# Kernel tuning notes

Measured on AMD Instinct MI355X. Metric: run time of the kernel, lower is better.

Reference implementation:

```python
import jax, jax.numpy as jnp
import numpy as np

B, S, D, H, F, E = 4, 1024, 1024, 16, 4096, 8
HD = D // H  # head dim


def setup_inputs() -> dict:
    key = jax.random.key(0)
    ks = jax.random.split(key, 8)
    p = lambda k, shp: jax.random.normal(k, shp, jnp.float32) * 0.02
    return {
        "x": jax.random.normal(ks[0], (B, S, D), jnp.float32),
        "mask": jnp.ones((B, S), jnp.int32),
        "in_proj_w": p(ks[1], (3 * D, D)),
        "in_proj_b": jnp.zeros((3 * D,), jnp.float32),
        "out_proj_w": p(ks[2], (D, D)),
        "out_proj_b": jnp.zeros((D,), jnp.float32),
        "ln1_g": jnp.ones((D,), jnp.float32),
        "ln1_b": jnp.zeros((D,), jnp.float32),
        "ln2_g": jnp.ones((D,), jnp.float32),
        "ln2_b": jnp.zeros((D,), jnp.float32),
        "gate_w": p(ks[3], (E, D)),
        "gate_b": jnp.zeros((E,), jnp.float32),
        "w1": p(ks[4], (E, F, D)),
        "b1": jnp.zeros((E, F), jnp.float32),
        "w2": p(ks[5], (E, D, F)),
        "b2": jnp.zeros((E, D), jnp.float32),
    }


def _layernorm(x, g, b, eps=1e-5):
    m = x.mean(-1, keepdims=True)
    v = ((x - m) ** 2).mean(-1, keepdims=True)
    return (x - m) / jnp.sqrt(v + eps) * g + b


def _mha(x, key_pad, in_proj_w, in_proj_b, out_proj_w, out_proj_b):
    # combined QKV projection as in torch nn.MultiheadAttention
    qkv = x @ in_proj_w.T + in_proj_b  # (B,S,3D)
    q, k, v = jnp.split(qkv, 3, axis=-1)
    def heads(t):
        return t.reshape(B, S, H, HD).transpose(0, 2, 1, 3)  # (B,H,S,HD)
    q, k, v = heads(q), heads(k), heads(v)
    scores = jnp.einsum("bhqd,bhkd->bhqk", q, k) / jnp.sqrt(jnp.float32(HD))
    scores = jnp.where(key_pad[:, None, None, :], -1e30, scores)
    attn = jax.nn.softmax(scores, axis=-1)
    out = jnp.einsum("bhqk,bhkd->bhqd", attn, v)  # (B,H,S,HD)
    out = out.transpose(0, 2, 1, 3).reshape(B, S, D)
    return out @ out_proj_w.T + out_proj_b


def _moe(x, gate_w, gate_b, w1, b1, w2, b2):
    logits = x @ gate_w.T + gate_b            # (B,S,E)
    probs = jax.nn.softmax(logits, axis=-1)
    # dense all-expert FFN (faithful to original: every expert computed)
    h = jax.nn.relu(jnp.einsum("bsd,efd->bsef", x, w1) + b1)   # (B,S,E,F)
    all_out = jnp.einsum("bsef,edf->bsed", h, w2) + b2          # (B,S,E,D)
    top_vals, top_idx = jax.lax.top_k(probs, 2)                 # (B,S,2)
    weights = top_vals / (top_vals.sum(-1, keepdims=True) + 1e-9)
    sel = jnp.take_along_axis(all_out, top_idx[..., None], axis=2)  # (B,S,2,D)
    return (sel * weights[..., None]).sum(axis=2)


def reference(x, mask, in_proj_w, in_proj_b, out_proj_w, out_proj_b,
              ln1_g, ln1_b, ln2_g, ln2_b, gate_w, gate_b, w1, b1, w2, b2):
    key_pad = mask == 0  # (B,S) bool
    attn_out = _mha(x, key_pad, in_proj_w, in_proj_b, out_proj_w, out_proj_b)
    x1 = _layernorm(x + attn_out, ln1_g, ln1_b)
    ff = _moe(x1, gate_w, gate_b, w1, b1, w2, b2)
    return _layernorm(x1 + ff, ln2_g, ln2_b)
```

## Files before the change

### kernel.cpp

```cpp
#include <hip/hip_runtime.h>

typedef __attribute__((ext_vector_type(8))) short bf16x8;
typedef __attribute__((ext_vector_type(4))) float f32x4;

#define DEV __device__ __forceinline__

static constexpr int Bb = 4, Sq = 1024, Dd = 1024, Hh = 16, HDd = 64, Ff = 4096, Ee = 8;
static constexpr int Nn = Bb * Sq;
static constexpr int TD = 3 * Dd;
static constexpr int PMAX = 2 * Nn + Ee * 128;

DEV unsigned short f2bf(float x) {
  union { float f; unsigned u; } c; c.f = x;
  unsigned r = c.u + 0x7FFFu + ((c.u >> 16) & 1u);
  return (unsigned short)(r >> 16);
}

typedef const __attribute__((address_space(1))) unsigned int* gas_t;
typedef __attribute__((address_space(3))) unsigned int* las_t;
DEV void gload16(const void* g, void* l) {
  __builtin_amdgcn_global_load_lds((gas_t)g, (las_t)l, 16, 0, 0);
}

__global__ __launch_bounds__(256) void cvt_kernel(const float* __restrict__ in,
                                                  unsigned short* __restrict__ out) {
  int i = blockIdx.x * 256 + threadIdx.x;
  const float4 a = *(const float4*)(in + (size_t)i * 8);
  const float4 b = *(const float4*)(in + (size_t)i * 8 + 4);
  union { uint4 u; unsigned short s[8]; } pk;
  pk.s[0] = f2bf(a.x); pk.s[1] = f2bf(a.y); pk.s[2] = f2bf(a.z); pk.s[3] = f2bf(a.w);
  pk.s[4] = f2bf(b.x); pk.s[5] = f2bf(b.y); pk.s[6] = f2bf(b.z); pk.s[7] = f2bf(b.w);
  *(uint4*)(out + (size_t)i * 8) = pk.u;
}

template <int EPI>
__global__ __launch_bounds__(256) void gemm_bt(
    const unsigned short* __restrict__ A, const unsigned short* __restrict__ Bw,
    const float* __restrict__ bias, void* __restrict__ o0, void* __restrict__ o1,
    void* __restrict__ o2, int M, int Ncols, int K,
    const int* __restrict__ poff) {
  int bx, by;
  {
    const int gx = gridDim.x, nwg = gx * gridDim.y;
    int orig = blockIdx.y * gx + blockIdx.x;
    int q = nwg >> 3, r = nwg & 7;
    int xcd = orig & 7, lin = orig >> 3;
    int wg = (xcd < r ? xcd * (q + 1) : r * (q + 1) + (xcd - r) * q) + lin;
    bx = wg % gx; by = wg / gx;
  }
  const int m0 = bx * 128;
  int e = 0;
  if constexpr (EPI >= 2) {
    if (m0 >= poff[Ee]) return;
#pragma unroll
    for (int k = 1; k < Ee; ++k) if (m0 >= poff[k]) e = k;
  } else {
    if (m0 >= M) return;
  }
  const int n0 = by * 128;
  const unsigned short* Bptr = Bw + (size_t)e * Ncols * K;
  const float* biasptr = bias + e * Ncols;

  __shared__ __align__(128) unsigned short As[3 * 128 * 32];
  __shared__ __align__(128) unsigned short Bs[3 * 128 * 32];

  const int tid = threadIdx.x;
  const int lane = tid & 63, wid = tid >> 6;
  const int wm = wid >> 1, wn = wid & 1;
  const int lr = lane & 15, lk = lane >> 4;

  const char* aSrc[2]; const char* bSrc[2];
  int dOff[2];
#pragma unroll
  for (int it = 0; it < 2; ++it) {
    int b = it * 4096 + tid * 16;
    int r = b >> 6;
    int colb = (b & 63) ^ (((r >> 1) & 3) << 4);
    aSrc[it] = (const char*)(A + (size_t)(m0 + r) * K) + colb;
    bSrc[it] = (const char*)(Bptr + (size_t)(n0 + r) * K) + colb;
    dOff[it] = it * 4096 + wid * 1024;
  }
  int aOff[4], bOff[4];
#pragma unroll
  for (int i = 0; i < 4; ++i) {
    int ra = wm * 64 + i * 16 + lr;
    aOff[i] = ra * 32 + ((lk ^ ((ra >> 1) & 3)) << 3);
    int rb = wn * 64 + i * 16 + lr;
    bOff[i] = rb * 32 + ((lk ^ ((rb >> 1) & 3)) << 3);
  }

  auto STAGE = [&](int t, int buf) {
#pragma unroll
    for (int it = 0; it < 2; ++it) {
      gload16(aSrc[it] + (size_t)t * 64, (char*)As + buf * 8192 + dOff[it]);
      gload16(bSrc[it] + (size_t)t * 64, (char*)Bs + buf * 8192 + dOff[it]);
    }
  };

  f32x4 acc[4][4] = {};
  const int NT = K >> 5;

  STAGE(0, 0);
  STAGE(1, 1);
  int cb = 0;
  int sb = 2;
  for (int t = 0; t < NT; ++t) {
    if (t + 1 < NT) asm volatile("s_waitcnt vmcnt(4)" ::: "memory");
    else            asm volatile("s_waitcnt vmcnt(0)" ::: "memory");
    __builtin_amdgcn_sched_barrier(0);
    __builtin_amdgcn_s_barrier();
    __builtin_amdgcn_sched_barrier(0);
    if (t + 2 < NT) STAGE(t + 2, sb);
    const unsigned short* Ab = As + cb * 4096;
    const unsigned short* Bb2 = Bs + cb * 4096;
    bf16x8 af[4], bfv[4];
#pragma unroll
    for (int mi = 0; mi < 4; ++mi) af[mi] = *(const bf16x8*)&Ab[aOff[mi]];
#pragma unroll
    for (int ni = 0; ni < 4; ++ni) bfv[ni] = *(const bf16x8*)&Bb2[bOff[ni]];
#pragma unroll
    for (int mi = 0; mi < 4; ++mi)
#pragma unroll
      for (int ni = 0; ni < 4; ++ni)
        acc[mi][ni] = __builtin_amdgcn_mfma_f32_16x16x32_bf16(af[mi], bfv[ni], acc[mi][ni], 0, 0, 0);
    cb = (cb == 2) ? 0 : cb + 1;
    sb = (sb == 2) ? 0 : sb + 1;
  }

#pragma unroll
  for (int ni = 0; ni < 4; ++ni) {
    const int col = n0 + wn * 64 + ni * 16 + lr;
    const float bv = biasptr[col];
#pragma unroll
    for (int mi = 0; mi < 4; ++mi) {
#pragma unroll
      for (int i = 0; i < 4; ++i) {
        const int mloc = wm * 64 + mi * 16 + lk * 4 + i;
        float v = acc[mi][ni][i] + bv;
        if constexpr (EPI == 0) {
          int t = m0 + mloc;
          int which = col >> 10, jj = col & 1023, hh = jj >> 6, hd = jj & 63;
          int bb = t >> 10, s = t & 1023;
          unsigned short* dst = (which == 0) ? (unsigned short*)o0
                              : (which == 1) ? (unsigned short*)o1 : (unsigned short*)o2;
          dst[((size_t)(bb * Hh + hh) * Sq + s) * HDd + hd] = f2bf(v);
        } else if constexpr (EPI == 1) {
          ((float*)o0)[(size_t)(m0 + mloc) * Dd + col] = v;
        } else if constexpr (EPI == 2) {
          ((unsigned short*)o0)[(size_t)(m0 + mloc) * Ff + col] = f2bf(fmaxf(v, 0.f));
        } else {
          ((float*)o0)[(size_t)(m0 + mloc) * Dd + col] = v;
        }
      }
    }
  }
}

__global__ __launch_bounds__(256) void attn_kernel(
    const unsigned short* __restrict__ qb, const unsigned short* __restrict__ kb,
    const unsigned short* __restrict__ vb, const int* __restrict__ mask,
    unsigned short* __restrict__ attnb) {
  const int qt = blockIdx.x, h = blockIdx.y, b = blockIdx.z;
  const unsigned short* Q = qb + (size_t)(b * Hh + h) * Sq * HDd;
  const unsigned short* Kg = kb + (size_t)(b * Hh + h) * Sq * HDd;
  const unsigned short* Vg = vb + (size_t)(b * Hh + h) * Sq * HDd;

  __shared__ unsigned short Qs[64 * 72], Ks[64 * 72], Vt[64 * 72], Ps[64 * 72];
  __shared__ float Ssm[64 * 65];
  __shared__ float mS[64], lS[64], aS[64];
  __shared__ int mk[64];

  const int tid = threadIdx.x, lane = tid & 63, wid = tid >> 6;
  const int lr = lane & 15, lk = lane >> 4;

#pragma unroll
  for (int it = 0; it < 2; ++it) {
    int c = tid + it * 256; int r = c >> 3, kc = (c & 7) * 8;
    *(uint4*)&Qs[r * 72 + kc] = *(const uint4*)(Q + (size_t)(qt * 64 + r) * 64 + kc);
  }
  if (tid < 64) { mS[tid] = -1e30f; lS[tid] = 0.f; }

  f32x4 oacc[4] = {};

  for (int kt = 0; kt < 16; ++kt) {
    __syncthreads();
#pragma unroll
    for (int it = 0; it < 2; ++it) {
      int c = tid + it * 256; int r = c >> 3, kc = (c & 7) * 8;
      *(uint4*)&Ks[r * 72 + kc] = *(const uint4*)(Kg + (size_t)(kt * 64 + r) * 64 + kc);
    }
    {
      int kk = tid >> 2, hg = (tid & 3) * 16;
      union { uint4 u[2]; unsigned short s[16]; } tv;
      tv.u[0] = *(const uint4*)(Vg + (size_t)(kt * 64 + kk) * 64 + hg);
      tv.u[1] = *(const uint4*)(Vg + (size_t)(kt * 64 + kk) * 64 + hg + 8);
#pragma unroll
      for (int j = 0; j < 16; ++j) Vt[(hg + j) * 72 + kk] = tv.s[j];
    }
    if (tid < 64) mk[tid] = mask[b * Sq + kt * 64 + tid];
    __syncthreads();

    f32x4 sacc[4] = {};
#pragma unroll
    for (int ks = 0; ks < 2; ++ks) {
      bf16x8 aq = *(const bf16x8*)&Qs[(wid * 16 + lr) * 72 + ks * 32 + lk * 8];
#pragma unroll
      for (int ni = 0; ni < 4; ++ni) {
        bf16x8 bk = *(const bf16x8*)&Ks[(ni * 16 + lr) * 72 + ks * 32 + lk * 8];
        sacc[ni] = __builtin_amdgcn_mfma_f32_16x16x32_bf16(aq, bk, sacc[ni], 0, 0, 0);
      }
    }
#pragma unroll
    for (int ni = 0; ni < 4; ++ni)
#pragma unroll
      for (int i = 0; i < 4; ++i) {
        int r = wid * 16 + lk * 4 + i, cc = ni * 16 + lr;
        float v = sacc[ni][i] * 0.125f;
        if (mk[cc] == 0) v = -1e30f;
        Ssm[r * 65 + cc] = v;
      }
    __syncthreads();
    {
      int r = tid >> 2, cg = (tid & 3) * 16;
      float xv[16];
#pragma unroll
      for (int j = 0; j < 16; ++j) xv[j] = Ssm[r * 65 + cg + j];
      float mx = xv[0];
#pragma unroll
      for (int j = 1; j < 16; ++j) mx = fmaxf(mx, xv[j]);
      mx = fmaxf(mx, __shfl_xor(mx, 1));
      mx = fmaxf(mx, __shfl_xor(mx, 2));
      float mprev = mS[r];
      float mnew = fmaxf(mprev, mx);
      float sum = 0.f;
      union { uint4 u[2]; unsigned short s[16]; } pb;
#pragma unroll
      for (int j = 0; j < 16; ++j) {
        float pv = expf(xv[j] - mnew);
        sum += pv; pb.s[j] = f2bf(pv);
      }
      sum += __shfl_xor(sum, 1);
      sum += __shfl_xor(sum, 2);
      *(uint4*)&Ps[r * 72 + cg] = pb.u[0];
      *(uint4*)&Ps[r * 72 + cg + 8] = pb.u[1];
      if ((tid & 3) == 0) {
        float alpha = expf(mprev - mnew);
        mS[r] = mnew; aS[r] = alpha; lS[r] = lS[r] * alpha + sum;
      }
    }
    __syncthreads();
#pragma unroll
    for (int ni = 0; ni < 4; ++ni)
#pragma unroll
      for (int i = 0; i < 4; ++i)
        oacc[ni][i] *= aS[wid * 16 + lk * 4 + i];
#pragma unroll
    for (int ks = 0; ks < 2; ++ks) {
      bf16x8 ap = *(const bf16x8*)&Ps[(wid * 16 + lr) * 72 + ks * 32 + lk * 8];
#pragma unroll
      for (int ni = 0; ni < 4; ++ni) {
        bf16x8 bv = *(const bf16x8*)&Vt[(ni * 16 + lr) * 72 + ks * 32 + lk * 8];
        oacc[ni] = __builtin_amdgcn_mfma_f32_16x16x32_bf16(ap, bv, oacc[ni], 0, 0, 0);
      }
    }
  }
  __syncthreads();
#pragma unroll
  for (int ni = 0; ni < 4; ++ni)
#pragma unroll
    for (int i = 0; i < 4; ++i) {
      int r = wid * 16 + lk * 4 + i;
      int q = qt * 64 + r;
      float v = oacc[ni][i] / lS[r];
      attnb[((size_t)(b * Sq + q)) * Dd + h * 64 + ni * 16 + lr] = f2bf(v);
    }
}

__global__ __launch_bounds__(256) void ln_kernel(
    const float* __restrict__ a, const float* __restrict__ b2,
    const float* __restrict__ g, const float* __restrict__ beta,
    float* __restrict__ outf, unsigned short* __restrict__ outb) {
  const int t = blockIdx.x, tid = threadIdx.x;
  float4 v = *(const float4*)(a + (size_t)t * Dd + tid * 4);
  {
    float4 u = *(const float4*)(b2 + (size_t)t * Dd + tid * 4);
    v.x += u.x; v.y += u.y; v.z += u.z; v.w += u.w;
  }
  const int lane = tid & 63, wid = tid >> 6;
  float s = v.x + v.y + v.z + v.w;
  for (int sh = 1; sh < 64; sh <<= 1) s += __shfl_xor(s, sh);
  __shared__ float red[4], red2[4];
  if (lane == 0) red[wid] = s;
  __syncthreads();
  float mean = (red[0] + red[1] + red[2] + red[3]) * (1.f / Dd);
  float dx = v.x - mean, dy = v.y - mean, dz = v.z - mean, dw = v.w - mean;
  float q = dx * dx + dy * dy + dz * dz + dw * dw;
  for (int sh = 1; sh < 64; sh <<= 1) q += __shfl_xor(q, sh);
  if (lane == 0) red2[wid] = q;
  __syncthreads();
  float var = (red2[0] + red2[1] + red2[2] + red2[3]) * (1.f / Dd);
  float rstd = rsqrtf(var + 1e-5f);
  float4 gg = *(const float4*)(g + tid * 4);
  float4 bb = *(const float4*)(beta + tid * 4);
  float4 o;
  o.x = dx * rstd * gg.x + bb.x;
  o.y = dy * rstd * gg.y + bb.y;
  o.z = dz * rstd * gg.z + bb.z;
  o.w = dw * rstd * gg.w + bb.w;
  if (outf) *(float4*)(outf + (size_t)t * Dd + tid * 4) = o;
  if (outb) {
    ushort4 pk; pk.x = f2bf(o.x); pk.y = f2bf(o.y); pk.z = f2bf(o.z); pk.w = f2bf(o.w);
    *(ushort4*)(outb + (size_t)t * Dd + tid * 4) = pk;
  }
}

__global__ __launch_bounds__(256) void ln2_kernel(
    const float* __restrict__ x1f, const float* __restrict__ ffp,
    const int* __restrict__ inv, const float* __restrict__ wtok,
    const float* __restrict__ g, const float* __restrict__ beta,
    float* __restrict__ out) {
  const int t = blockIdx.x, tid = threadIdx.x;
  const int i0 = inv[2 * t], i1 = inv[2 * t + 1];
  const float w0 = wtok[2 * t], w1 = wtok[2 * t + 1];
  float4 v = *(const float4*)(x1f + (size_t)t * Dd + tid * 4);
  float4 u0 = *(const float4*)(ffp + (size_t)i0 * Dd + tid * 4);
  float4 u1 = *(const float4*)(ffp + (size_t)i1 * Dd + tid * 4);
  v.x += w0 * u0.x + w1 * u1.x; v.y += w0 * u0.y + w1 * u1.y;
  v.z += w0 * u0.z + w1 * u1.z; v.w += w0 * u0.w + w1 * u1.w;
  const int lane = tid & 63, wid = tid >> 6;
  float s = v.x + v.y + v.z + v.w;
  for (int sh = 1; sh < 64; sh <<= 1) s += __shfl_xor(s, sh);
  __shared__ float red[4], red2[4];
  if (lane == 0) red[wid] = s;
  __syncthreads();
  float mean = (red[0] + red[1] + red[2] + red[3]) * (1.f / Dd);
  float dx = v.x - mean, dy = v.y - mean, dz = v.z - mean, dw = v.w - mean;
  float q = dx * dx + dy * dy + dz * dz + dw * dw;
  for (int sh = 1; sh < 64; sh <<= 1) q += __shfl_xor(q, sh);
  if (lane == 0) red2[wid] = q;
  __syncthreads();
  float var = (red2[0] + red2[1] + red2[2] + red2[3]) * (1.f / Dd);
  float rstd = rsqrtf(var + 1e-5f);
  float4 gg = *(const float4*)(g + tid * 4);
  float4 bb = *(const float4*)(beta + tid * 4);
  float4 o;
  o.x = dx * rstd * gg.x + bb.x;
  o.y = dy * rstd * gg.y + bb.y;
  o.z = dz * rstd * gg.z + bb.z;
  o.w = dw * rstd * gg.w + bb.w;
  *(float4*)(out + (size_t)t * Dd + tid * 4) = o;
}

__global__ __launch_bounds__(256) void route_kernel(
    const float* __restrict__ x1f, const float* __restrict__ gw, const float* __restrict__ gb,
    int* __restrict__ cnt, int* __restrict__ tokslot, float* __restrict__ wtok) {
  __shared__ float gws[Ee * Dd];
  const int tid = threadIdx.x;
#pragma unroll
  for (int it = 0; it < 8; ++it) {
    int idx = (tid + it * 256) * 4;
    *(float4*)&gws[idx] = *(const float4*)(gw + idx);
  }
  __syncthreads();
  const int lane = tid & 63, wid = tid >> 6;
  for (int it = 0; it < 16; ++it) {
    int t = blockIdx.x * 64 + wid * 16 + it;
    float acc[Ee] = {};
    for (int i = 0; i < 16; ++i) {
      float xv = x1f[(size_t)t * Dd + i * 64 + lane];
#pragma unroll
      for (int e = 0; e < Ee; ++e) acc[e] += xv * gws[e * Dd + i * 64 + lane];
    }
#pragma unroll
    for (int e = 0; e < Ee; ++e) {
      float vv = acc[e];
      for (int sh = 1; sh < 64; sh <<= 1) vv += __shfl_xor(vv, sh);
      acc[e] = vv;
    }
    if (lane == 0) {
      float lg[Ee];
#pragma unroll
      for (int e = 0; e < Ee; ++e) lg[e] = acc[e] + gb[e];
      float m = lg[0];
#pragma unroll
      for (int e = 1; e < Ee; ++e) m = fmaxf(m, lg[e]);
      float p[Ee], ssum = 0.f;
#pragma unroll
      for (int e = 0; e < Ee; ++e) { p[e] = expf(lg[e] - m); ssum += p[e]; }
      int e0 = 0;
#pragma unroll
      for (int e = 1; e < Ee; ++e) if (p[e] > p[e0]) e0 = e;
      int e1 = -1;
#pragma unroll
      for (int e = 0; e < Ee; ++e) {
        if (e == e0) continue;
        if (e1 < 0 || p[e] > p[e1]) e1 = e;
      }
      float v0 = p[e0] / ssum, v1 = p[e1] / ssum;
      float wsum = v0 + v1 + 1e-9f;
      wtok[t * 2] = v0 / wsum; wtok[t * 2 + 1] = v1 / wsum;
      int p0 = atomicAdd(&cnt[e0], 1);
      tokslot[e0 * Nn + p0] = t * 2;
      int p1 = atomicAdd(&cnt[e1], 1);
      tokslot[e1 * Nn + p1] = t * 2 + 1;
    }
  }
}

__global__ void offsets_kernel(const int* __restrict__ cnt, int* __restrict__ poff) {
  if (threadIdx.x == 0) {
    int s = 0;
    for (int e = 0; e < Ee; ++e) { poff[e] = s; s += (cnt[e] + 127) & ~127; }
    poff[Ee] = s;
  }
}

__global__ __launch_bounds__(256) void pack_kernel(
    const unsigned short* __restrict__ x1b, const int* __restrict__ tokslot,
    const int* __restrict__ cnt, const int* __restrict__ poff,
    unsigned short* __restrict__ xg, int* __restrict__ inv) {
  const int tid = threadIdx.x;
  const int g = blockIdx.x * 8 + (tid >> 5);
  const int l = tid & 31;
  if (g >= poff[Ee]) return;
  int e = 0;
#pragma unroll
  for (int k = 1; k < Ee; ++k) if (g >= poff[k]) e = k;
  const int pos = g - poff[e];
  uint4* dst = (uint4*)(xg + (size_t)g * Dd);
  if (pos < cnt[e]) {
    const int ent = tokslot[e * Nn + pos];
    if (l == 0) inv[ent] = g;
    const uint4* src = (const uint4*)(x1b + (size_t)(ent >> 1) * Dd);
#pragma unroll
    for (int j = 0; j < 4; ++j) dst[l + j * 32] = src[l + j * 32];
  } else {
    const uint4 z = make_uint4(0, 0, 0, 0);
#pragma unroll
    for (int j = 0; j < 4; ++j) dst[l + j * 32] = z;
  }
}

extern "C" void kernel_launch(void* const* d_in, const int* in_sizes, int n_in,
                              void* d_out, int out_size, void* d_ws, size_t ws_size,
                              hipStream_t stream) {
  const float* x   = (const float*)d_in[0];
  const int*   msk = (const int*)d_in[1];
  const float* ipw = (const float*)d_in[2];
  const float* ipb = (const float*)d_in[3];
  const float* opw = (const float*)d_in[4];
  const float* opb = (const float*)d_in[5];
  const float* g1  = (const float*)d_in[6];
  const float* be1 = (const float*)d_in[7];
  const float* g2  = (const float*)d_in[8];
  const float* be2 = (const float*)d_in[9];
  const float* gw  = (const float*)d_in[10];
  const float* gb  = (const float*)d_in[11];
  const float* w1  = (const float*)d_in[12];
  const float* b1  = (const float*)d_in[13];
  const float* w2  = (const float*)d_in[14];
  const float* b2  = (const float*)d_in[15];
  float* out = (float*)d_out;

  char* p = (char*)d_ws;
  auto carve = [&](size_t bytes) { char* r = p; p += (bytes + 255) & ~(size_t)255; return r; };
  unsigned short* xb   = (unsigned short*)carve((size_t)Nn * Dd * 2);
  unsigned short* qb   = (unsigned short*)carve((size_t)Nn * Dd * 2);
  unsigned short* kb   = (unsigned short*)carve((size_t)Nn * Dd * 2);
  unsigned short* vb   = (unsigned short*)carve((size_t)Nn * Dd * 2);
  float* proj          = (float*)carve((size_t)Nn * Dd * 4);
  float* x1f           = (float*)carve((size_t)Nn * Dd * 4);
  unsigned short* x1b  = (unsigned short*)carve((size_t)Nn * Dd * 2);
  unsigned short* xg   = (unsigned short*)carve((size_t)PMAX * Dd * 2);
  float* ffp           = (float*)carve((size_t)PMAX * Dd * 4);
  unsigned short* hbuf = (unsigned short*)carve((size_t)PMAX * Ff * 2);
  unsigned short* wbuf = (unsigned short*)carve((size_t)Ee * Ff * Dd * 2);
  int* cnt             = (int*)carve(64);
  int* poff            = (int*)carve(64);
  int* tokslot         = (int*)carve((size_t)Ee * Nn * 4);
  float* wtok          = (float*)carve((size_t)2 * Nn * 4);
  int* inv             = (int*)carve((size_t)2 * Nn * 4);
  unsigned short* attnb = xb;

  cvt_kernel<<<Nn * Dd / 2048, 256, 0, stream>>>(x, xb);
  cvt_kernel<<<TD * Dd / 2048, 256, 0, stream>>>(ipw, wbuf);
  gemm_bt<0><<<dim3(Nn / 128, TD / 128), 256, 0, stream>>>(
      xb, wbuf, ipb, qb, kb, vb, Nn, TD, Dd, nullptr);
  attn_kernel<<<dim3(Sq / 64, Hh, Bb), 256, 0, stream>>>(qb, kb, vb, msk, attnb);
  cvt_kernel<<<Dd * Dd / 2048, 256, 0, stream>>>(opw, wbuf);
  gemm_bt<1><<<dim3(Nn / 128, Dd / 128), 256, 0, stream>>>(
      attnb, wbuf, opb, proj, nullptr, nullptr, Nn, Dd, Dd, nullptr);
  ln_kernel<<<Nn, 256, 0, stream>>>(x, proj, g1, be1, x1f, x1b);
  hipMemsetAsync(cnt, 0, 64, stream);
  route_kernel<<<Nn / 64, 256, 0, stream>>>(x1f, gw, gb, cnt, tokslot, wtok);
  offsets_kernel<<<1, 64, 0, stream>>>(cnt, poff);
  pack_kernel<<<PMAX / 8, 256, 0, stream>>>(x1b, tokslot, cnt, poff, xg, inv);
  cvt_kernel<<<Ee * Ff * Dd / 2048, 256, 0, stream>>>(w1, wbuf);
  gemm_bt<2><<<dim3(PMAX / 128, Ff / 128), 256, 0, stream>>>(
      xg, wbuf, b1, hbuf, nullptr, nullptr, PMAX, Ff, Dd, poff);
  cvt_kernel<<<Ee * Dd * Ff / 2048, 256, 0, stream>>>(w2, wbuf);
  gemm_bt<3><<<dim3(PMAX / 128, Dd / 128), 256, 0, stream>>>(
      hbuf, wbuf, b2, ffp, nullptr, nullptr, PMAX, Dd, Ff, poff);
  ln2_kernel<<<Nn, 256, 0, stream>>>(x1f, ffp, inv, wtok, g2, be2, out);
}
```

Before: 627.5 us.

## Use 256-row tiles with 512-thread blocks for the MoE expert GEMMs

Adds a new gemm256 kernel for the two grouped expert GEMMs. It uses 256-row M tiles with 256- or 128-wide N tiles, a 64-wide K step, double-buffered LDS and 8 waves per block, in place of the 128x128 tile kernel with K step 32. Per-expert padding goes from 128 to 256 rows to match. This is meant to raise data reuse per block and cut the number of barriers and loads per MFMA, at the cost of more padding rows, fewer blocks and higher LDS and register use per block.

```diff
diff --git a/kernel.cpp b/kernel.cpp
--- a/kernel.cpp
+++ b/kernel.cpp
@@ -8,7 +8,7 @@
 static constexpr int Bb = 4, Sq = 1024, Dd = 1024, Hh = 16, HDd = 64, Ff = 4096, Ee = 8;
 static constexpr int Nn = Bb * Sq;
 static constexpr int TD = 3 * Dd;
-static constexpr int PMAX = 2 * Nn + Ee * 128;
+static constexpr int PMAX = 2 * Nn + Ee * 256;
 
 DEV unsigned short f2bf(float x) {
   union { float f; unsigned u; } c; c.f = x;
@@ -33,12 +33,19 @@
   *(uint4*)(out + (size_t)i * 8) = pk.u;
 }
 
-template <int EPI>
-__global__ __launch_bounds__(256) void gemm_bt(
+template <int EPI, int TN>
+__global__ __launch_bounds__(512) void gemm256(
     const unsigned short* __restrict__ A, const unsigned short* __restrict__ Bw,
-    const float* __restrict__ bias, void* __restrict__ o0, void* __restrict__ o1,
-    void* __restrict__ o2, int M, int Ncols, int K,
-    const int* __restrict__ poff) {
+    const float* __restrict__ bias, void* __restrict__ o0,
+    int Ncols, int K, const int* __restrict__ poff) {
+  constexpr int NW_N = TN / 64;
+  constexpr int NW_M = 8 / NW_N;
+  constexpr int RM = 256 / NW_M;
+  constexpr int MI = RM / 16;
+  constexpr int NB = TN / 64;
+  constexpr int ASZ = 256 * 64;
+  constexpr int BSZ = TN * 64;
+
   int bx, by;
   {
     const int gx = gridDim.x, nwg = gx * gridDim.y;
@@ -48,18 +55,136 @@
     int wg = (xcd < r ? xcd * (q + 1) : r * (q + 1) + (xcd - r) * q) + lin;
     bx = wg % gx; by = wg / gx;
   }
-  const int m0 = bx * 128;
+  const int m0 = bx * 256;
+  if (m0 >= poff[Ee]) return;
   int e = 0;
-  if constexpr (EPI >= 2) {
-    if (m0 >= poff[Ee]) return;
-#pragma unroll
-    for (int k = 1; k < Ee; ++k) if (m0 >= poff[k]) e = k;
-  } else {
-    if (m0 >= M) return;
-  }
-  const int n0 = by * 128;
+#pragma unroll
+  for (int k = 1; k < Ee; ++k) if (m0 >= poff[k]) e = k;
+  const int n0 = by * TN;
   const unsigned short* Bptr = Bw + (size_t)e * Ncols * K;
   const float* biasptr = bias + e * Ncols;
+
+  __shared__ __align__(128) unsigned short As[2 * ASZ];
+  __shared__ __align__(128) unsigned short Bs[2 * BSZ];
+
+  const int tid = threadIdx.x;
+  const int lane = tid & 63, wid = tid >> 6;
+  const int wm = wid / NW_N, wn = wid % NW_N;
+  const int lr = lane & 15, lk = lane >> 4;
+
+  const char* aSrc[4]; const char* bSrc[NB];
+  int aDstOff[4], bDstOff[NB];
+#pragma unroll
+  for (int it = 0; it < 4; ++it) {
+    int b = it * 8192 + tid * 16;
+    int r = b >> 7;
+    int colb = (b & 127) ^ ((r & 7) << 4);
+    aSrc[it] = (const char*)(A + (size_t)(m0 + r) * K) + colb;
+    aDstOff[it] = it * 8192 + wid * 1024;
+  }
+#pragma unroll
+  for (int it = 0; it < NB; ++it) {
+    int b = it * 8192 + tid * 16;
+    int r = b >> 7;
+    int colb = (b & 127) ^ ((r & 7) << 4);
+    bSrc[it] = (const char*)(Bptr + (size_t)(n0 + r) * K) + colb;
+    bDstOff[it] = it * 8192 + wid * 1024;
+  }
+  int aOff[2][MI], bOff[2][4];
+#pragma unroll
+  for (int ks = 0; ks < 2; ++ks) {
+#pragma unroll
+    for (int i = 0; i < MI; ++i) {
+      int ra = wm * RM + i * 16 + lr;
+      aOff[ks][i] = ra * 64 + (((ks * 4 + lk) ^ (ra & 7)) << 3);
+    }
+#pragma unroll
+    for (int i = 0; i < 4; ++i) {
+      int rb = wn * 64 + i * 16 + lr;
+      bOff[ks][i] = rb * 64 + (((ks * 4 + lk) ^ (rb & 7)) << 3);
+    }
+  }
+
+  f32x4 acc[MI][4] = {};
+  const int NT = K >> 6;
+
+  auto STAGE = [&](int t, int buf) {
+#pragma unroll
+    for (int it = 0; it < 4; ++it)
+      gload16(aSrc[it] + (size_t)t * 128, (char*)As + buf * (ASZ * 2) + aDstOff[it]);
+#pragma unroll
+    for (int it = 0; it < NB; ++it)
+      gload16(bSrc[it] + (size_t)t * 128, (char*)Bs + buf * (BSZ * 2) + bDstOff[it]);
+  };
+
+  STAGE(0, 0);
+  for (int t = 0; t < NT; ++t) {
+    __builtin_amdgcn_s_barrier();
+    __builtin_amdgcn_sched_barrier(0);
+    if (t + 1 < NT) {
+      STAGE(t + 1, (t + 1) & 1);
+      if constexpr (TN == 256) asm volatile("s_waitcnt vmcnt(8)" ::: "memory");
+      else                     asm volatile("s_waitcnt vmcnt(6)" ::: "memory");
+    } else {
+      asm volatile("s_waitcnt vmcnt(0)" ::: "memory");
+    }
+    __builtin_amdgcn_sched_barrier(0);
+    __builtin_amdgcn_s_barrier();
+    __builtin_amdgcn_sched_barrier(0);
+    const unsigned short* Ab = As + (t & 1) * ASZ;
+    const unsigned short* Bb2 = Bs + (t & 1) * BSZ;
+#pragma unroll
+    for (int ks = 0; ks < 2; ++ks) {
+      bf16x8 af[MI], bfv[4];
+#pragma unroll
+      for (int mi = 0; mi < MI; ++mi) af[mi] = *(const bf16x8*)&Ab[aOff[ks][mi]];
+#pragma unroll
+      for (int ni = 0; ni < 4; ++ni) bfv[ni] = *(const bf16x8*)&Bb2[bOff[ks][ni]];
+#pragma unroll
+      for (int mi = 0; mi < MI; ++mi)
+#pragma unroll
+        for (int ni = 0; ni < 4; ++ni)
+          acc[mi][ni] = __builtin_amdgcn_mfma_f32_16x16x32_bf16(af[mi], bfv[ni], acc[mi][ni], 0, 0, 0);
+    }
+  }
+
+#pragma unroll
+  for (int ni = 0; ni < 4; ++ni) {
+    const int col = n0 + wn * 64 + ni * 16 + lr;
+    const float bv = biasptr[col];
+#pragma unroll
+    for (int mi = 0; mi < MI; ++mi) {
+#pragma unroll
+      for (int i = 0; i < 4; ++i) {
+        const int grow = m0 + wm * RM + mi * 16 + lk * 4 + i;
+        float v = acc[mi][ni][i] + bv;
+        if constexpr (EPI == 2) {
+          ((unsigned short*)o0)[(size_t)grow * Ff + col] = f2bf(fmaxf(v, 0.f));
+        } else {
+          ((float*)o0)[(size_t)grow * Dd + col] = v;
+        }
+      }
+    }
+  }
+}
+
+template <int EPI>
+__global__ __launch_bounds__(256) void gemm_bt(
+    const unsigned short* __restrict__ A, const unsigned short* __restrict__ Bw,
+    const float* __restrict__ bias, void* __restrict__ o0, void* __restrict__ o1,
+    void* __restrict__ o2, int M, int Ncols, int K) {
+  int bx, by;
+  {
+    const int gx = gridDim.x, nwg = gx * gridDim.y;
+    int orig = blockIdx.y * gx + blockIdx.x;
+    int q = nwg >> 3, r = nwg & 7;
+    int xcd = orig & 7, lin = orig >> 3;
+    int wg = (xcd < r ? xcd * (q + 1) : r * (q + 1) + (xcd - r) * q) + lin;
+    bx = wg % gx; by = wg / gx;
+  }
+  const int m0 = bx * 128;
+  if (m0 >= M) return;
+  const int n0 = by * 128;
 
   __shared__ __align__(128) unsigned short As[3 * 128 * 32];
   __shared__ __align__(128) unsigned short Bs[3 * 128 * 32];
@@ -77,7 +202,7 @@
     int r = b >> 6;
     int colb = (b & 63) ^ (((r >> 1) & 3) << 4);
     aSrc[it] = (const char*)(A + (size_t)(m0 + r) * K) + colb;
-    bSrc[it] = (const char*)(Bptr + (size_t)(n0 + r) * K) + colb;
+    bSrc[it] = (const char*)(Bw + (size_t)(n0 + r) * K) + colb;
     dOff[it] = it * 4096 + wid * 1024;
   }
   int aOff[4], bOff[4];
@@ -102,8 +227,7 @@
 
   STAGE(0, 0);
   STAGE(1, 1);
-  int cb = 0;
-  int sb = 2;
+  int cb = 0, sb = 2;
   for (int t = 0; t < NT; ++t) {
     if (t + 1 < NT) asm volatile("s_waitcnt vmcnt(4)" ::: "memory");
     else            asm volatile("s_waitcnt vmcnt(0)" ::: "memory");
@@ -130,7 +254,7 @@
 #pragma unroll
   for (int ni = 0; ni < 4; ++ni) {
     const int col = n0 + wn * 64 + ni * 16 + lr;
-    const float bv = biasptr[col];
+    const float bv = bias[col];
 #pragma unroll
     for (int mi = 0; mi < 4; ++mi) {
 #pragma unroll
@@ -144,10 +268,6 @@
           unsigned short* dst = (which == 0) ? (unsigned short*)o0
                               : (which == 1) ? (unsigned short*)o1 : (unsigned short*)o2;
           dst[((size_t)(bb * Hh + hh) * Sq + s) * HDd + hd] = f2bf(v);
-        } else if constexpr (EPI == 1) {
-          ((float*)o0)[(size_t)(m0 + mloc) * Dd + col] = v;
-        } else if constexpr (EPI == 2) {
-          ((unsigned short*)o0)[(size_t)(m0 + mloc) * Ff + col] = f2bf(fmaxf(v, 0.f));
         } else {
           ((float*)o0)[(size_t)(m0 + mloc) * Dd + col] = v;
         }
@@ -410,7 +530,7 @@
 __global__ void offsets_kernel(const int* __restrict__ cnt, int* __restrict__ poff) {
   if (threadIdx.x == 0) {
     int s = 0;
-    for (int e = 0; e < Ee; ++e) { poff[e] = s; s += (cnt[e] + 127) & ~127; }
+    for (int e = 0; e < Ee; ++e) { poff[e] = s; s += (cnt[e] + 255) & ~255; }
     poff[Ee] = s;
   }
 }
@@ -485,21 +605,21 @@
   cvt_kernel<<<Nn * Dd / 2048, 256, 0, stream>>>(x, xb);
   cvt_kernel<<<TD * Dd / 2048, 256, 0, stream>>>(ipw, wbuf);
   gemm_bt<0><<<dim3(Nn / 128, TD / 128), 256, 0, stream>>>(
-      xb, wbuf, ipb, qb, kb, vb, Nn, TD, Dd, nullptr);
+      xb, wbuf, ipb, qb, kb, vb, Nn, TD, Dd);
   attn_kernel<<<dim3(Sq / 64, Hh, Bb), 256, 0, stream>>>(qb, kb, vb, msk, attnb);
   cvt_kernel<<<Dd * Dd / 2048, 256, 0, stream>>>(opw, wbuf);
   gemm_bt<1><<<dim3(Nn / 128, Dd / 128), 256, 0, stream>>>(
-      attnb, wbuf, opb, proj, nullptr, nullptr, Nn, Dd, Dd, nullptr);
+      attnb, wbuf, opb, proj, nullptr, nullptr, Nn, Dd, Dd);
   ln_kernel<<<Nn, 256, 0, stream>>>(x, proj, g1, be1, x1f, x1b);
   hipMemsetAsync(cnt, 0, 64, stream);
   route_kernel<<<Nn / 64, 256, 0, stream>>>(x1f, gw, gb, cnt, tokslot, wtok);
   offsets_kernel<<<1, 64, 0, stream>>>(cnt, poff);
   pack_kernel<<<PMAX / 8, 256, 0, stream>>>(x1b, tokslot, cnt, poff, xg, inv);
   cvt_kernel<<<Ee * Ff * Dd / 2048, 256, 0, stream>>>(w1, wbuf);
-  gemm_bt<2><<<dim3(PMAX / 128, Ff / 128), 256, 0, stream>>>(
-      xg, wbuf, b1, hbuf, nullptr, nullptr, PMAX, Ff, Dd, poff);
+  gemm256<2, 256><<<dim3(PMAX / 256, Ff / 256), 512, 0, stream>>>(
+      xg, wbuf, b1, hbuf, Ff, Dd, poff);
   cvt_kernel<<<Ee * Dd * Ff / 2048, 256, 0, stream>>>(w2, wbuf);
-  gemm_bt<3><<<dim3(PMAX / 128, Dd / 128), 256, 0, stream>>>(
-      hbuf, wbuf, b2, ffp, nullptr, nullptr, PMAX, Dd, Ff, poff);
+  gemm256<3, 128><<<dim3(PMAX / 256, Dd / 128), 512, 0, stream>>>(
+      hbuf, wbuf, b2, ffp, Dd, Ff, poff);
   ln2_kernel<<<Nn, 256, 0, stream>>>(x1f, ffp, inv, wtok, g2, be2, out);
 }
```

Result: slower. 700.2 us (+11.6%).

## Add 256x256 8-wave expert up-projection GEMM and fuse LN1 with routing

Applied to the files above, without the earlier changes.

Replaces the expert up-projection GEMM with a new 512-thread kernel using 256x256 tiles, K=64 double-buffered LDS stages and four interleaved load/compute phases with wave priority boosts. Expert padding is raised to 256 rows to match the larger tile. Separately, the gating/top-2 routing is folded into the first layernorm kernel so x1 is not re-read by a separate route kernel. The larger tile raises data reuse but increases LDS and register pressure and adds padding rows of wasted work.

```diff
diff --git a/kernel.cpp b/kernel.cpp
--- a/kernel.cpp
+++ b/kernel.cpp
@@ -8,7 +8,7 @@
 static constexpr int Bb = 4, Sq = 1024, Dd = 1024, Hh = 16, HDd = 64, Ff = 4096, Ee = 8;
 static constexpr int Nn = Bb * Sq;
 static constexpr int TD = 3 * Dd;
-static constexpr int PMAX = 2 * Nn + Ee * 128;
+static constexpr int PMAX = 2 * Nn + Ee * 256;
 
 DEV unsigned short f2bf(float x) {
   union { float f; unsigned u; } c; c.f = x;
@@ -33,24 +33,155 @@
   *(uint4*)(out + (size_t)i * 8) = pk.u;
 }
 
+DEV void xcd_swz(int& bx, int& by, int gx, int gy) {
+  const int nwg = gx * gy;
+  int orig = by * gx + bx;
+  int q = nwg >> 3, r = nwg & 7;
+  int xcd = orig & 7, lin = orig >> 3;
+  int wg = (xcd < r ? xcd * (q + 1) : r * (q + 1) + (xcd - r) * q) + lin;
+  bx = wg % gx; by = wg / gx;
+}
+
+__global__ __launch_bounds__(512) void gemm8p_up(
+    const unsigned short* __restrict__ A, const unsigned short* __restrict__ Bw,
+    const float* __restrict__ bias, unsigned short* __restrict__ o0,
+    const int* __restrict__ poff) {
+  constexpr int K = Dd;
+  constexpr int NT = K / 64;
+  int bx = blockIdx.x, by = blockIdx.y;
+  xcd_swz(bx, by, gridDim.x, gridDim.y);
+  const int m0 = bx * 256;
+  if (m0 >= poff[Ee]) return;
+  int e = 0;
+#pragma unroll
+  for (int k = 1; k < Ee; ++k) if (m0 >= poff[k]) e = k;
+  const int n0 = by * 256;
+  const unsigned short* Bptr = Bw + (size_t)e * Ff * K;
+  const float* biasptr = bias + e * Ff;
+
+  __shared__ __align__(128) unsigned short As[2 * 256 * 64];
+  __shared__ __align__(128) unsigned short Bs[2 * 256 * 64];
+
+  const int tid = threadIdx.x;
+  const int lane = tid & 63, wid = tid >> 6;
+  const int aw = wid & 1, bw = wid >> 1;
+  const int lr = lane & 15, lk = lane >> 4;
+
+  const char* aS[2][2]; const char* bS[2][2]; int dOf[2];
+#pragma unroll
+  for (int it = 0; it < 2; ++it) {
+    int b = it * 8192 + tid * 16;
+    int r = b >> 7;
+    int colb = (b & 127) ^ ((r & 7) << 4);
+#pragma unroll
+    for (int h = 0; h < 2; ++h) {
+      aS[h][it] = (const char*)(A + (size_t)(m0 + h * 128 + r) * K) + colb;
+      bS[h][it] = (const char*)(Bptr + (size_t)(n0 + h * 128 + r) * K) + colb;
+    }
+    dOf[it] = it * 8192 + wid * 1024;
+  }
+  int aO[2][2][4], bO[2][2][2];
+#pragma unroll
+  for (int h = 0; h < 2; ++h)
+#pragma unroll
+    for (int ks = 0; ks < 2; ++ks) {
+#pragma unroll
+      for (int mi = 0; mi < 4; ++mi) {
+        int ra = h * 128 + aw * 64 + mi * 16 + lr;
+        aO[h][ks][mi] = ra * 64 + (((ks * 4 + lk) ^ (ra & 7)) << 3);
+      }
+#pragma unroll
+      for (int ni = 0; ni < 2; ++ni) {
+        int rb = h * 128 + bw * 32 + ni * 16 + lr;
+        bO[h][ks][ni] = rb * 64 + (((ks * 4 + lk) ^ (rb & 7)) << 3);
+      }
+    }
+
+  f32x4 acc[4][4][2] = {};
+
+  auto ST_A = [&](int t, int h) {
+    int buf = t & 1;
+#pragma unroll
+    for (int it = 0; it < 2; ++it)
+      gload16(aS[h][it] + (size_t)t * 128, (char*)As + buf * 32768 + h * 16384 + dOf[it]);
+  };
+  auto ST_B = [&](int t, int h) {
+    int buf = t & 1;
+#pragma unroll
+    for (int it = 0; it < 2; ++it)
+      gload16(bS[h][it] + (size_t)t * 128, (char*)Bs + buf * 32768 + h * 16384 + dOf[it]);
+  };
+
+  ST_A(0, 0); ST_B(0, 0); ST_B(0, 1); ST_A(0, 1);
+
+  for (int t = 0; t < NT; ++t) {
+    const unsigned short* Ab = As + (t & 1) * 16384;
+    const unsigned short* Bb = Bs + (t & 1) * 16384;
+#pragma unroll
+    for (int p = 0; p < 4; ++p) {
+      const int ah = p >> 1, bh = p & 1;
+      if (t + 1 < NT) {
+        if (p == 0)      ST_A(t + 1, 0);
+        else if (p == 1) ST_B(t + 1, 0);
+        else if (p == 2) ST_B(t + 1, 1);
+        else             ST_A(t + 1, 1);
+        asm volatile("s_waitcnt vmcnt(6)" ::: "memory");
+      } else {
+        if (p == 0)      asm volatile("s_waitcnt vmcnt(4)" ::: "memory");
+        else if (p == 1) asm volatile("s_waitcnt vmcnt(2)" ::: "memory");
+        else             asm volatile("s_waitcnt vmcnt(0)" ::: "memory");
+      }
+      __builtin_amdgcn_sched_barrier(0);
+      asm volatile("s_barrier" ::: "memory");
+      __builtin_amdgcn_sched_barrier(0);
+      bf16x8 af[2][4], bf[2][2];
+#pragma unroll
+      for (int ks = 0; ks < 2; ++ks) {
+#pragma unroll
+        for (int mi = 0; mi < 4; ++mi) af[ks][mi] = *(const bf16x8*)&Ab[aO[ah][ks][mi]];
+#pragma unroll
+        for (int ni = 0; ni < 2; ++ni) bf[ks][ni] = *(const bf16x8*)&Bb[bO[bh][ks][ni]];
+      }
+      __builtin_amdgcn_s_setprio(1);
+#pragma unroll
+      for (int ks = 0; ks < 2; ++ks)
+#pragma unroll
+        for (int mi = 0; mi < 4; ++mi)
+#pragma unroll
+          for (int ni = 0; ni < 2; ++ni)
+            acc[p][mi][ni] = __builtin_amdgcn_mfma_f32_16x16x32_bf16(af[ks][mi], bf[ks][ni], acc[p][mi][ni], 0, 0, 0);
+      __builtin_amdgcn_s_setprio(0);
+    }
+  }
+
+#pragma unroll
+  for (int p = 0; p < 4; ++p)
+#pragma unroll
+    for (int ni = 0; ni < 2; ++ni) {
+      const int col = n0 + (p & 1) * 128 + bw * 32 + ni * 16 + lr;
+      const float bv = biasptr[col];
+#pragma unroll
+      for (int mi = 0; mi < 4; ++mi)
+#pragma unroll
+        for (int i = 0; i < 4; ++i) {
+          const int row = m0 + (p >> 1) * 128 + aw * 64 + mi * 16 + lk * 4 + i;
+          float v = acc[p][mi][ni][i] + bv;
+          o0[(size_t)row * Ff + col] = f2bf(fmaxf(v, 0.f));
+        }
+    }
+}
+
 template <int EPI>
 __global__ __launch_bounds__(256) void gemm_bt(
     const unsigned short* __restrict__ A, const unsigned short* __restrict__ Bw,
     const float* __restrict__ bias, void* __restrict__ o0, void* __restrict__ o1,
     void* __restrict__ o2, int M, int Ncols, int K,
     const int* __restrict__ poff) {
-  int bx, by;
-  {
-    const int gx = gridDim.x, nwg = gx * gridDim.y;
-    int orig = blockIdx.y * gx + blockIdx.x;
-    int q = nwg >> 3, r = nwg & 7;
-    int xcd = orig & 7, lin = orig >> 3;
-    int wg = (xcd < r ? xcd * (q + 1) : r * (q + 1) + (xcd - r) * q) + lin;
-    bx = wg % gx; by = wg / gx;
-  }
+  int bx = blockIdx.x, by = blockIdx.y;
+  xcd_swz(bx, by, gridDim.x, gridDim.y);
   const int m0 = bx * 128;
   int e = 0;
-  if constexpr (EPI >= 2) {
+  if constexpr (EPI == 3) {
     if (m0 >= poff[Ee]) return;
 #pragma unroll
     for (int k = 1; k < Ee; ++k) if (m0 >= poff[k]) e = k;
@@ -102,8 +233,7 @@
 
   STAGE(0, 0);
   STAGE(1, 1);
-  int cb = 0;
-  int sb = 2;
+  int cb = 0, sb = 2;
   for (int t = 0; t < NT; ++t) {
     if (t + 1 < NT) asm volatile("s_waitcnt vmcnt(4)" ::: "memory");
     else            asm volatile("s_waitcnt vmcnt(0)" ::: "memory");
@@ -146,8 +276,6 @@
           dst[((size_t)(bb * Hh + hh) * Sq + s) * HDd + hd] = f2bf(v);
         } else if constexpr (EPI == 1) {
           ((float*)o0)[(size_t)(m0 + mloc) * Dd + col] = v;
-        } else if constexpr (EPI == 2) {
-          ((unsigned short*)o0)[(size_t)(m0 + mloc) * Ff + col] = f2bf(fmaxf(v, 0.f));
         } else {
           ((float*)o0)[(size_t)(m0 + mloc) * Dd + col] = v;
         }
@@ -276,10 +404,12 @@
     }
 }
 
-__global__ __launch_bounds__(256) void ln_kernel(
+__global__ __launch_bounds__(256) void ln1_route_kernel(
     const float* __restrict__ a, const float* __restrict__ b2,
     const float* __restrict__ g, const float* __restrict__ beta,
-    float* __restrict__ outf, unsigned short* __restrict__ outb) {
+    const float* __restrict__ gw, const float* __restrict__ gb,
+    float* __restrict__ outf, unsigned short* __restrict__ outb,
+    int* __restrict__ cnt, int* __restrict__ tokslot, float* __restrict__ wtok) {
   const int t = blockIdx.x, tid = threadIdx.x;
   float4 v = *(const float4*)(a + (size_t)t * Dd + tid * 4);
   {
@@ -290,6 +420,7 @@
   float s = v.x + v.y + v.z + v.w;
   for (int sh = 1; sh < 64; sh <<= 1) s += __shfl_xor(s, sh);
   __shared__ float red[4], red2[4];
+  __shared__ float gred[4 * Ee];
   if (lane == 0) red[wid] = s;
   __syncthreads();
   float mean = (red[0] + red[1] + red[2] + red[3]) * (1.f / Dd);
@@ -301,16 +432,58 @@
   float var = (red2[0] + red2[1] + red2[2] + red2[3]) * (1.f / Dd);
   float rstd = rsqrtf(var + 1e-5f);
   float4 gg = *(const float4*)(g + tid * 4);
-  float4 bb = *(const float4*)(beta + tid * 4);
+  float4 bbv = *(const float4*)(beta + tid * 4);
   float4 o;
-  o.x = dx * rstd * gg.x + bb.x;
-  o.y = dy * rstd * gg.y + bb.y;
-  o.z = dz * rstd * gg.z + bb.z;
-  o.w = dw * rstd * gg.w + bb.w;
-  if (outf) *(float4*)(outf + (size_t)t * Dd + tid * 4) = o;
-  if (outb) {
+  o.x = dx * rstd * gg.x + bbv.x;
+  o.y = dy * rstd * gg.y + bbv.y;
+  o.z = dz * rstd * gg.z + bbv.z;
+  o.w = dw * rstd * gg.w + bbv.w;
+  *(float4*)(outf + (size_t)t * Dd + tid * 4) = o;
+  {
     ushort4 pk; pk.x = f2bf(o.x); pk.y = f2bf(o.y); pk.z = f2bf(o.z); pk.w = f2bf(o.w);
     *(ushort4*)(outb + (size_t)t * Dd + tid * 4) = pk;
+  }
+  float gacc[Ee];
+#pragma unroll
+  for (int e = 0; e < Ee; ++e) {
+    float4 gv = *(const float4*)(gw + (size_t)e * Dd + tid * 4);
+    gacc[e] = o.x * gv.x + o.y * gv.y + o.z * gv.z + o.w * gv.w;
+  }
+#pragma unroll
+  for (int e = 0; e < Ee; ++e)
+    for (int sh = 1; sh < 64; sh <<= 1) gacc[e] += __shfl_xor(gacc[e], sh);
+  if (lane == 0) {
+#pragma unroll
+    for (int e = 0; e < Ee; ++e) gred[wid * Ee + e] = gacc[e];
+  }
+  __syncthreads();
+  if (tid == 0) {
+    float lg[Ee];
+#pragma unroll
+    for (int e = 0; e < Ee; ++e)
+      lg[e] = gred[e] + gred[Ee + e] + gred[2 * Ee + e] + gred[3 * Ee + e] + gb[e];
+    float m = lg[0];
+#pragma unroll
+    for (int e = 1; e < Ee; ++e) m = fmaxf(m, lg[e]);
+    float p[Ee], ssum = 0.f;
+#pragma unroll
+    for (int e = 0; e < Ee; ++e) { p[e] = expf(lg[e] - m); ssum += p[e]; }
+    int e0 = 0;
+#pragma unroll
+    for (int e = 1; e < Ee; ++e) if (p[e] > p[e0]) e0 = e;
+    int e1 = -1;
+#pragma unroll
+    for (int e = 0; e < Ee; ++e) {
+      if (e == e0) continue;
+      if (e1 < 0 || p[e] > p[e1]) e1 = e;
+    }
+    float v0 = p[e0] / ssum, v1 = p[e1] / ssum;
+    float wsum = v0 + v1 + 1e-9f;
+    wtok[t * 2] = v0 / wsum; wtok[t * 2 + 1] = v1 / wsum;
+    int p0 = atomicAdd(&cnt[e0], 1);
+    tokslot[e0 * Nn + p0] = t * 2;
+    int p1 = atomicAdd(&cnt[e1], 1);
+    tokslot[e1 * Nn + p1] = t * 2 + 1;
   }
 }
 
@@ -351,66 +524,10 @@
   *(float4*)(out + (size_t)t * Dd + tid * 4) = o;
 }
 
-__global__ __launch_bounds__(256) void route_kernel(
-    const float* __restrict__ x1f, const float* __restrict__ gw, const float* __restrict__ gb,
-    int* __restrict__ cnt, int* __restrict__ tokslot, float* __restrict__ wtok) {
-  __shared__ float gws[Ee * Dd];
-  const int tid = threadIdx.x;
-#pragma unroll
-  for (int it = 0; it < 8; ++it) {
-    int idx = (tid + it * 256) * 4;
-    *(float4*)&gws[idx] = *(const float4*)(gw + idx);
-  }
-  __syncthreads();
-  const int lane = tid & 63, wid = tid >> 6;
-  for (int it = 0; it < 16; ++it) {
-    int t = blockIdx.x * 64 + wid * 16 + it;
-    float acc[Ee] = {};
-    for (int i = 0; i < 16; ++i) {
-      float xv = x1f[(size_t)t * Dd + i * 64 + lane];
-#pragma unroll
-      for (int e = 0; e < Ee; ++e) acc[e] += xv * gws[e * Dd + i * 64 + lane];
-    }
-#pragma unroll
-    for (int e = 0; e < Ee; ++e) {
-      float vv = acc[e];
-      for (int sh = 1; sh < 64; sh <<= 1) vv += __shfl_xor(vv, sh);
-      acc[e] = vv;
-    }
-    if (lane == 0) {
-      float lg[Ee];
-#pragma unroll
-      for (int e = 0; e < Ee; ++e) lg[e] = acc[e] + gb[e];
-      float m = lg[0];
-#pragma unroll
-      for (int e = 1; e < Ee; ++e) m = fmaxf(m, lg[e]);
-      float p[Ee], ssum = 0.f;
-#pragma unroll
-      for (int e = 0; e < Ee; ++e) { p[e] = expf(lg[e] - m); ssum += p[e]; }
-      int e0 = 0;
-#pragma unroll
-      for (int e = 1; e < Ee; ++e) if (p[e] > p[e0]) e0 = e;
-      int e1 = -1;
-#pragma unroll
-      for (int e = 0; e < Ee; ++e) {
-        if (e == e0) continue;
-        if (e1 < 0 || p[e] > p[e1]) e1 = e;
-      }
-      float v0 = p[e0] / ssum, v1 = p[e1] / ssum;
-      float wsum = v0 + v1 + 1e-9f;
-      wtok[t * 2] = v0 / wsum; wtok[t * 2 + 1] = v1 / wsum;
-      int p0 = atomicAdd(&cnt[e0], 1);
-      tokslot[e0 * Nn + p0] = t * 2;
-      int p1 = atomicAdd(&cnt[e1], 1);
-      tokslot[e1 * Nn + p1] = t * 2 + 1;
-    }
-  }
-}
-
 __global__ void offsets_kernel(const int* __restrict__ cnt, int* __restrict__ poff) {
   if (threadIdx.x == 0) {
     int s = 0;
-    for (int e = 0; e < Ee; ++e) { poff[e] = s; s += (cnt[e] + 127) & ~127; }
+    for (int e = 0; e < Ee; ++e) { poff[e] = s; s += (cnt[e] + 255) & ~255; }
     poff[Ee] = s;
   }
 }
@@ -490,14 +607,13 @@
   cvt_kernel<<<Dd * Dd / 2048, 256, 0, stream>>>(opw, wbuf);
   gemm_bt<1><<<dim3(Nn / 128, Dd / 128), 256, 0, stream>>>(
       attnb, wbuf, opb, proj, nullptr, nullptr, Nn, Dd, Dd, nullptr);
-  ln_kernel<<<Nn, 256, 0, stream>>>(x, proj, g1, be1, x1f, x1b);
   hipMemsetAsync(cnt, 0, 64, stream);
-  route_kernel<<<Nn / 64, 256, 0, stream>>>(x1f, gw, gb, cnt, tokslot, wtok);
+  ln1_route_kernel<<<Nn, 256, 0, stream>>>(x, proj, g1, be1, gw, gb,
+                                           x1f, x1b, cnt, tokslot, wtok);
   offsets_kernel<<<1, 64, 0, stream>>>(cnt, poff);
   pack_kernel<<<PMAX / 8, 256, 0, stream>>>(x1b, tokslot, cnt, poff, xg, inv);
   cvt_kernel<<<Ee * Ff * Dd / 2048, 256, 0, stream>>>(w1, wbuf);
-  gemm_bt<2><<<dim3(PMAX / 128, Ff / 128), 256, 0, stream>>>(
-      xg, wbuf, b1, hbuf, nullptr, nullptr, PMAX, Ff, Dd, poff);
+  gemm8p_up<<<dim3(PMAX / 256, Ff / 256), 512, 0, stream>>>(xg, wbuf, b1, hbuf, poff);
   cvt_kernel<<<Ee * Dd * Ff / 2048, 256, 0, stream>>>(w2, wbuf);
   gemm_bt<3><<<dim3(PMAX / 128, Dd / 128), 256, 0, stream>>>(
       hbuf, wbuf, b2, ffp, nullptr, nullptr, PMAX, Dd, Ff, poff);
```

After: 614.0 us. -2.2%, faster.
